# Kernel optimization log

Measured on AMD Instinct MI355X. Metric: run time of the kernel, lower is better.

## Reference

```python
import jax, jax.numpy as jnp
import numpy as np

B = 8          # batch_size
N = 2048       # N_particles
D_SP = 2       # spatial dims
D = 16         # D_SP + hidden_dim
K = 32         # max_num_neighbors
R = 0.08       # neighbor_radius
DT = 0.01      # leapfrog step
BIG = 1e9


def setup_inputs() -> dict:
    key = jax.random.key(0)
    ks = jax.random.split(key, 8)
    H, C = 64, 32
    # node state: small random hidden features, deterministic disk positions
    x = jax.random.normal(ks[0], (B * N, D), dtype=jnp.float32) * 0.001
    i = jnp.arange(N, dtype=jnp.float32)
    golden = jnp.pi * (3.0 - jnp.sqrt(5.0))
    theta = i * golden
    r = 0.6 * jnp.sqrt((i + 0.5) / N)
    pos = jnp.stack([r * jnp.cos(theta), r * jnp.sin(theta)], axis=1)  # [N,2]
    pos = jnp.tile(pos, (B, 1)) + 0.01 * jax.random.normal(ks[1], (B * N, 2), dtype=jnp.float32)
    x = x.at[:, :D_SP].set(pos)
    W1 = jax.random.normal(ks[2], (2 * D, H), dtype=jnp.float32) * (1.0 / np.sqrt(2 * D))
    b1 = jnp.zeros((H,), jnp.float32)
    W2 = jax.random.normal(ks[3], (H, C), dtype=jnp.float32) * (1.0 / np.sqrt(H))
    b2 = jnp.zeros((C,), jnp.float32)
    Wout = jax.random.normal(ks[4], (C, 1), dtype=jnp.float32) * (1.0 / np.sqrt(C))
    bout = jnp.zeros((1,), jnp.float32)
    batch = jnp.repeat(jnp.arange(B, dtype=jnp.int64), N)
    return {"x": x, "W1": W1, "b1": b1, "W2": W2, "b2": b2,
            "Wout": Wout, "bout": bout, "batch": batch, "steps": 2}


def reference(x, W1, b1, W2, b2, Wout, bout, batch, steps):
    Bn, Df = x.shape
    Bc = int(np.asarray(batch)[-1]) + 1      # batch is contiguous blocks
    Nn = Bn // Bc
    eye = jnp.eye(Nn, dtype=x.dtype) * BIG   # no self-loops (loop=False)

    def hamiltonian(xv):
        xb = xv.reshape(Bc, Nn, Df)
        pos = xb[:, :, :D_SP]                              # [B,N,2]
        # radius_graph: pairwise sq-dist per simulation, capped at K neighbors
        d2 = jnp.sum((pos[:, :, None, :] - pos[:, None, :, :]) ** 2, axis=-1)  # [B,N,N]
        d2 = d2 + eye
        negd, idx = jax.lax.top_k(-d2, K)                  # K nearest per node
        valid = (-negd) < (R * R)                          # [B,N,K]
        # gather neighbor states (HNNConv message on concat(x_i, x_j))
        xj = xb[jnp.arange(Bc)[:, None, None], idx]        # [B,N,K,D]
        xi = jnp.broadcast_to(xb[:, :, None, :], xj.shape)
        m = jnp.tanh(jnp.concatenate([xi, xj], axis=-1) @ W1 + b1)  # [B,N,K,H]
        m = m @ W2 + b2                                    # [B,N,K,C]
        m = jnp.where(valid[..., None], m, 0.0)
        agg = m.sum(axis=2)                                # sum aggregation [B,N,C]
        h = agg @ Wout + bout                              # per-node Hamiltonian [B,N,1]
        return h.sum()

    for _ in range(int(steps)):
        dHdx = jax.grad(hamiltonian)(x)
        x = x - DT * dHdx
    return x
```

## Files before the change

### kernel.cpp

```cpp
#include <hip/hip_runtime.h>
#include <cstdint>
#include <cstddef>

#define BB   8
#define NN   2048
#define DD   16
#define HHH  64
#define KK   32
#define CAP  96
#define DT_C 0.01f
#define R2_C (0.08f * 0.08f)
#define CEXP (-2.885390081777927f)

#define WPB   16
#define BLOCK (WPB * 64)

__device__ __forceinline__ float dist2(float px, float py, float qx, float qy) {
    float dx = __fsub_rn(px, qx);
    float dy = __fsub_rn(py, qy);
    return __fadd_rn(__fmul_rn(dx, dx), __fmul_rn(dy, dy));
}

__device__ __forceinline__ int mbcnt64(unsigned long long m) {
    return (int)__builtin_amdgcn_mbcnt_hi(
        (unsigned)(m >> 32), __builtin_amdgcn_mbcnt_lo((unsigned)m, 0u));
}

template <bool FIRST>
__global__ __launch_bounds__(BLOCK) void k_neighbors(
    const float* __restrict__ x, const float* __restrict__ pos,
    const float* __restrict__ W1,
    unsigned short* __restrict__ nbr, int* __restrict__ cntArr,
    float* __restrict__ cutArr,
    float* __restrict__ Aplane, float* __restrict__ Dplane) {
    __shared__ float sPos[2 * NN];
    __shared__ float sW1[2 * DD * HHH];
    __shared__ float2 sDJ[WPB][CAP];

    int tid = threadIdx.x;
    int w = tid >> 6, lane = tid & 63;
    int p = blockIdx.x * WPB + w;
    int pl = p & (NN - 1);
    int bbase = (p >> 11) << 11;

    if (FIRST) {
        for (int t = tid; t < 2 * NN; t += BLOCK)
            sPos[t] = x[(size_t)(bbase + (t >> 1)) * DD + (t & 1)];
    } else {
        for (int t = tid; t < 2 * NN; t += BLOCK) sPos[t] = pos[bbase * 2 + t];
    }
    for (int t = tid; t < 2 * DD * HHH; t += BLOCK) sW1[t] = W1[t];
    __syncthreads();

    float xv = (lane < DD) ? x[(size_t)p * DD + lane] : 0.f;
    float A = 0.f, Dv = 0.f;
#pragma unroll
    for (int f = 0; f < DD; f++) {
        float xf = __shfl(xv, f);
        A  = fmaf(xf, sW1[f * HHH + lane], A);
        Dv = fmaf(xf, sW1[(DD + f) * HHH + lane], Dv);
    }
    Aplane[((size_t)p << 6) + lane] = A;
    Dplane[((size_t)p << 6) + lane] = Dv;

    float px = sPos[2 * pl], py = sPos[2 * pl + 1];
    const float2* sPos2 = (const float2*)sPos;
    int cnt = 0;
    for (int c0 = 0; c0 < NN; c0 += 256) {
        float2 q[4];
#pragma unroll
        for (int u = 0; u < 4; ++u) q[u] = sPos2[c0 + (u << 6) + lane];
#pragma unroll
        for (int u = 0; u < 4; ++u) {
            int j = c0 + (u << 6) + lane;
            float d2 = dist2(px, py, q[u].x, q[u].y);
            bool hit = (d2 < R2_C) && (j != pl);
            unsigned long long m = __ballot(hit);
            int idx = cnt + mbcnt64(m & ((1ull << lane) - 1ull));
            if (hit && idx < CAP)
                sDJ[w][idx] = make_float2(d2, __uint_as_float((unsigned)j));
            cnt += (int)__popcll(m);
        }
    }
    if (cnt > CAP) cnt = CAP;
    __threadfence_block();

    float cutoff = R2_C;
    if (cnt > KK) {
        const float INF = 1e30f;
        if (cnt <= 64) {
            float v = (lane < cnt) ? sDJ[w][lane].x : INF;
#pragma unroll
            for (int k = 2; k <= 64; k <<= 1) {
#pragma unroll
                for (int j = k >> 1; j > 0; j >>= 1) {
                    float pv = __shfl_xor(v, j);
                    bool up = ((lane & k) == 0);
                    bool takeMin = (((lane & j) == 0) == up);
                    v = takeMin ? fminf(v, pv) : fmaxf(v, pv);
                }
            }
            cutoff = __shfl(v, KK - 1);
        } else {
            float e0 = (lane < cnt) ? sDJ[w][lane].x : INF;
            float e1 = (lane + 64 < cnt) ? sDJ[w][lane + 64].x : INF;
            int r0 = 0, q0 = 0, r1 = 0, q1 = 0;
            for (int k = 0; k < cnt; k++) {
                float val = sDJ[w][k].x;
                r0 += (val < e0); q0 += (val == e0);
                r1 += (val < e1); q1 += (val == e1);
            }
            bool c0 = (r0 <= KK - 1) && (r0 + q0 > KK - 1);
            bool c1 = (r1 <= KK - 1) && (r1 + q1 > KK - 1);
            float cand = c0 ? e0 : (c1 ? e1 : INF);
#pragma unroll
            for (int off = 32; off; off >>= 1) cand = fminf(cand, __shfl_xor(cand, off));
            cutoff = cand;
        }
    }
    if (lane == 0) { cutArr[p] = cutoff; cntArr[p] = cnt; }
    for (int c = lane; c < cnt; c += 64) {
        float2 e = sDJ[w][c];
        unsigned j = __float_as_uint(e.y);
        bool fwd = (e.x <= cutoff);
        nbr[(size_t)p * CAP + c] = (unsigned short)(j | (fwd ? 0x8000u : 0u));
    }
}

template <bool FIRST>
__global__ __launch_bounds__(BLOCK) void k_grad(
    const float* __restrict__ x, const float* __restrict__ pos,
    const float* __restrict__ cutArr, const int* __restrict__ cntArr,
    const unsigned short* __restrict__ nbr,
    const float* __restrict__ Aplane, const float* __restrict__ Dplane,
    const float* __restrict__ W1, const float* __restrict__ b1,
    const float* __restrict__ W2, const float* __restrict__ Wout,
    float* __restrict__ xOut, float* __restrict__ posOut) {
    __shared__ float sW1t[HHH * 33];
    __shared__ unsigned short sFwd[WPB][CAP];
    __shared__ unsigned short sRev[WPB][CAP];
    __shared__ float sS[WPB][128];
    __shared__ float sV[HHH];

    int tid = threadIdx.x;
    int w = tid >> 6, h = tid & 63;
    int p = blockIdx.x * WPB + w;
    int bbase = (p >> 11) << 11;

    for (int t = tid; t < 2 * DD * HHH; t += BLOCK) {
        int f = t >> 6, hh = t & 63;
        sW1t[hh * 33 + f] = W1[t];
    }
    if (tid < HHH) {
        float acc = 0.f;
        for (int c = 0; c < 32; c++) acc = fmaf(W2[tid * 32 + c], Wout[c], acc);
        sV[tid] = acc;
    }
    __syncthreads();

    float b1h = b1[h];
    float Apb = Aplane[((size_t)p << 6) + h] + b1h;
    float Dpb = Dplane[((size_t)p << 6) + h] + b1h;
    float vh4 = 4.f * sV[h];
    int cnt = cntArr[p];

    float px, py;
    if (FIRST) {
        float2 pp = *(const float2*)(x + (size_t)p * DD);
        px = pp.x; py = pp.y;
    } else {
        float2 pp = *(const float2*)(pos + (size_t)p * 2);
        px = pp.x; py = pp.y;
    }

    int mf = 0, mr = 0;
    for (int c0 = 0; c0 < cnt; c0 += 64) {
        int c = c0 + h;
        bool act = c < cnt;
        int cc = act ? c : cnt - 1;
        int jp = (int)nbr[(size_t)p * CAP + cc];
        int jl = jp & (NN - 1);
        float2 q;
        if (FIRST) q = *(const float2*)(x + (size_t)(bbase + jl) * DD);
        else       q = *(const float2*)(pos + (size_t)(bbase + jl) * 2);
        float d2 = dist2(px, py, q.x, q.y);
        float cutj = cutArr[bbase + jl];
        bool fwd = act && (jp & 0x8000);
        bool rev = act && (d2 <= cutj);
        unsigned long long mF = __ballot(fwd);
        int iF = mf + mbcnt64(mF & ((1ull << h) - 1ull));
        if (fwd) sFwd[w][iF] = (unsigned short)jl;
        mf += (int)__popcll(mF);
        unsigned long long mR = __ballot(rev);
        int iR = mr + mbcnt64(mR & ((1ull << h) - 1ull));
        if (rev) sRev[w][iR] = (unsigned short)jl;
        mr += (int)__popcll(mR);
    }
    __threadfence_block();

    const float* baseD = Dplane + ((size_t)bbase << 6);
    const float* baseA = Aplane + ((size_t)bbase << 6);
    float T1 = 0.f, T2 = 0.f;

    auto edgeF = [&](unsigned jl) {
        float dj = baseD[((size_t)jl << 6) + h];
        float z = Apb + dj;
        float a = __builtin_amdgcn_exp2f(CEXP * fabsf(z));
        float bb = 1.f + a;
        T1 += a * __builtin_amdgcn_rcpf(bb * bb);
    };
    auto edgeR = [&](unsigned jl) {
        float aj = baseA[((size_t)jl << 6) + h];
        float z = Dpb + aj;
        float a = __builtin_amdgcn_exp2f(CEXP * fabsf(z));
        float bb = 1.f + a;
        T2 += a * __builtin_amdgcn_rcpf(bb * bb);
    };

    {
        const unsigned short* L = sFwd[w];
        int c = 0;
        for (; c + 8 <= mf; c += 8) {
            int4 qw = *(const int4*)(L + c);
            unsigned w0 = (unsigned)__builtin_amdgcn_readfirstlane(qw.x);
            unsigned w1 = (unsigned)__builtin_amdgcn_readfirstlane(qw.y);
            unsigned w2 = (unsigned)__builtin_amdgcn_readfirstlane(qw.z);
            unsigned w3 = (unsigned)__builtin_amdgcn_readfirstlane(qw.w);
            edgeF(w0 & 0xffffu); edgeF(w0 >> 16);
            edgeF(w1 & 0xffffu); edgeF(w1 >> 16);
            edgeF(w2 & 0xffffu); edgeF(w2 >> 16);
            edgeF(w3 & 0xffffu); edgeF(w3 >> 16);
        }
        for (; c < mf; ++c)
            edgeF((unsigned)__builtin_amdgcn_readfirstlane((int)L[c]));
    }
    {
        const unsigned short* L = sRev[w];
        int c = 0;
        for (; c + 8 <= mr; c += 8) {
            int4 qw = *(const int4*)(L + c);
            unsigned w0 = (unsigned)__builtin_amdgcn_readfirstlane(qw.x);
            unsigned w1 = (unsigned)__builtin_amdgcn_readfirstlane(qw.y);
            unsigned w2 = (unsigned)__builtin_amdgcn_readfirstlane(qw.z);
            unsigned w3 = (unsigned)__builtin_amdgcn_readfirstlane(qw.w);
            edgeR(w0 & 0xffffu); edgeR(w0 >> 16);
            edgeR(w1 & 0xffffu); edgeR(w1 >> 16);
            edgeR(w2 & 0xffffu); edgeR(w2 >> 16);
            edgeR(w3 & 0xffffu); edgeR(w3 >> 16);
        }
        for (; c < mr; ++c)
            edgeR((unsigned)__builtin_amdgcn_readfirstlane((int)L[c]));
    }

    sS[w][h] = vh4 * T1;
    sS[w][64 + h] = vh4 * T2;
    __threadfence_block();

    float g = 0.f;
    if (h < 32) {
        const float* Sv = &sS[w][(h < 16) ? 0 : 64];
        float acc = 0.f;
        for (int hh = 0; hh < 64; hh++) acc = fmaf(sW1t[hh * 33 + h], Sv[hh], acc);
        g = acc;
    }
    float g2 = __shfl(g, (h + 16) & 63);
    if (h < DD) {
        float xn = x[(size_t)p * DD + h] - DT_C * (g + g2);
        xOut[(size_t)p * DD + h] = xn;
        if (h < 2) posOut[p * 2 + h] = xn;
    }
}

extern "C" void kernel_launch(void* const* d_in, const int* in_sizes, int n_in,
                              void* d_out, int out_size, void* d_ws, size_t ws_size,
                              hipStream_t stream) {
    const float* x0   = (const float*)d_in[0];
    const float* W1   = (const float*)d_in[1];
    const float* b1   = (const float*)d_in[2];
    const float* W2   = (const float*)d_in[3];
    const float* Wout = (const float*)d_in[5];
    float* out = (float*)d_out;

    float* ws   = (float*)d_ws;
    float* posA = ws;
    float* posB = posA + 32768;
    float* x1   = posB + 32768;
    float* Apl  = x1 + 262144;
    float* Dpl  = Apl + 16384 * 64;
    float* cut  = Dpl + 16384 * 64;
    int*   cnt  = (int*)(cut + 16384);
    unsigned short* nbr = (unsigned short*)(cnt + 16384);

    dim3 blk(BLOCK);
    const int NBLK = (BB * NN) / WPB;

    k_neighbors<true><<<NBLK, blk, 0, stream>>>(x0, nullptr, W1, nbr, cnt, cut, Apl, Dpl);
    k_grad<true><<<NBLK, blk, 0, stream>>>(x0, nullptr, cut, cnt, nbr, Apl, Dpl,
                                           W1, b1, W2, Wout, x1, posB);
    k_neighbors<false><<<NBLK, blk, 0, stream>>>(x1, posB, W1, nbr, cnt, cut, Apl, Dpl);
    k_grad<false><<<NBLK, blk, 0, stream>>>(x1, posB, cut, cnt, nbr, Apl, Dpl,
                                            W1, b1, W2, Wout, out, posA);
}
```

Baseline: 189.1 us.

## Swizzle block-to-batch mapping, vectorize position loads, batch gathers in edge loops

Blocks are remapped so consecutive block IDs cycle across the eight simulations, which spreads concurrent work over different batch slices of the A/D planes. The first-step position staging now loads float2 pairs instead of scalars. The edge loops in the gradient kernel are unrolled to 16 edges, with all 16 gathers issued before the exp/rcp math so more memory loads are in flight. The cost is higher register pressure, and the swizzle may reduce L2 locality for neighbour-plane reads.

```diff
diff --git a/kernel.cpp b/kernel.cpp
--- a/kernel.cpp
+++ b/kernel.cpp
@@ -24,6 +24,12 @@
 __device__ __forceinline__ int mbcnt64(unsigned long long m) {
     return (int)__builtin_amdgcn_mbcnt_hi(
         (unsigned)(m >> 32), __builtin_amdgcn_mbcnt_lo((unsigned)m, 0u));
+}
+
+__device__ __forceinline__ int swizzled_particle(int blk, int w, int& bbase) {
+    int vb = blk & 7, vi = blk >> 3;
+    bbase = vb << 11;
+    return bbase + vi * WPB + w;
 }
 
 template <bool FIRST>
@@ -39,13 +45,14 @@
 
     int tid = threadIdx.x;
     int w = tid >> 6, lane = tid & 63;
-    int p = blockIdx.x * WPB + w;
+    int bbase;
+    int p = swizzled_particle(blockIdx.x, w, bbase);
     int pl = p & (NN - 1);
-    int bbase = (p >> 11) << 11;
-
+
+    float2* sPos2w = (float2*)sPos;
     if (FIRST) {
-        for (int t = tid; t < 2 * NN; t += BLOCK)
-            sPos[t] = x[(size_t)(bbase + (t >> 1)) * DD + (t & 1)];
+        for (int t = tid; t < NN; t += BLOCK)
+            sPos2w[t] = *(const float2*)(x + (size_t)(bbase + t) * DD);
     } else {
         for (int t = tid; t < 2 * NN; t += BLOCK) sPos[t] = pos[bbase * 2 + t];
     }
@@ -137,15 +144,15 @@
     const float* __restrict__ W2, const float* __restrict__ Wout,
     float* __restrict__ xOut, float* __restrict__ posOut) {
     __shared__ float sW1t[HHH * 33];
-    __shared__ unsigned short sFwd[WPB][CAP];
-    __shared__ unsigned short sRev[WPB][CAP];
+    __shared__ alignas(16) unsigned short sFwd[WPB][CAP];
+    __shared__ alignas(16) unsigned short sRev[WPB][CAP];
     __shared__ float sS[WPB][128];
     __shared__ float sV[HHH];
 
     int tid = threadIdx.x;
     int w = tid >> 6, h = tid & 63;
-    int p = blockIdx.x * WPB + w;
-    int bbase = (p >> 11) << 11;
+    int bbase;
+    int p = swizzled_particle(blockIdx.x, w, bbase);
 
     for (int t = tid; t < 2 * DD * HHH; t += BLOCK) {
         int f = t >> 6, hh = t & 63;
@@ -202,55 +209,92 @@
     const float* baseA = Aplane + ((size_t)bbase << 6);
     float T1 = 0.f, T2 = 0.f;
 
-    auto edgeF = [&](unsigned jl) {
-        float dj = baseD[((size_t)jl << 6) + h];
-        float z = Apb + dj;
+    auto s2core = [&](float z) {
         float a = __builtin_amdgcn_exp2f(CEXP * fabsf(z));
         float bb = 1.f + a;
-        T1 += a * __builtin_amdgcn_rcpf(bb * bb);
+        return a * __builtin_amdgcn_rcpf(bb * bb);
     };
-    auto edgeR = [&](unsigned jl) {
-        float aj = baseA[((size_t)jl << 6) + h];
-        float z = Dpb + aj;
-        float a = __builtin_amdgcn_exp2f(CEXP * fabsf(z));
-        float bb = 1.f + a;
-        T2 += a * __builtin_amdgcn_rcpf(bb * bb);
-    };
+
+#define UNPACK8(Q0, Q1, U)                                            \
+    unsigned U[8];                                                    \
+    U[0] = (unsigned)__builtin_amdgcn_readfirstlane(Q0.x);            \
+    U[1] = (unsigned)__builtin_amdgcn_readfirstlane(Q0.y);            \
+    U[2] = (unsigned)__builtin_amdgcn_readfirstlane(Q0.z);            \
+    U[3] = (unsigned)__builtin_amdgcn_readfirstlane(Q0.w);            \
+    U[4] = (unsigned)__builtin_amdgcn_readfirstlane(Q1.x);            \
+    U[5] = (unsigned)__builtin_amdgcn_readfirstlane(Q1.y);            \
+    U[6] = (unsigned)__builtin_amdgcn_readfirstlane(Q1.z);            \
+    U[7] = (unsigned)__builtin_amdgcn_readfirstlane(Q1.w);
 
     {
         const unsigned short* L = sFwd[w];
         int c = 0;
+        for (; c + 16 <= mf; c += 16) {
+            int4 q0 = *(const int4*)(L + c);
+            int4 q1 = *(const int4*)(L + c + 8);
+            UNPACK8(q0, q1, u)
+            float d[16];
+#pragma unroll
+            for (int k = 0; k < 8; ++k) {
+                d[2 * k]     = baseD[((size_t)(u[k] & 0xffffu) << 6) + h];
+                d[2 * k + 1] = baseD[((size_t)(u[k] >> 16) << 6) + h];
+            }
+#pragma unroll
+            for (int k = 0; k < 16; ++k) T1 += s2core(Apb + d[k]);
+        }
         for (; c + 8 <= mf; c += 8) {
-            int4 qw = *(const int4*)(L + c);
-            unsigned w0 = (unsigned)__builtin_amdgcn_readfirstlane(qw.x);
-            unsigned w1 = (unsigned)__builtin_amdgcn_readfirstlane(qw.y);
-            unsigned w2 = (unsigned)__builtin_amdgcn_readfirstlane(qw.z);
-            unsigned w3 = (unsigned)__builtin_amdgcn_readfirstlane(qw.w);
-            edgeF(w0 & 0xffffu); edgeF(w0 >> 16);
-            edgeF(w1 & 0xffffu); edgeF(w1 >> 16);
-            edgeF(w2 & 0xffffu); edgeF(w2 >> 16);
-            edgeF(w3 & 0xffffu); edgeF(w3 >> 16);
-        }
-        for (; c < mf; ++c)
-            edgeF((unsigned)__builtin_amdgcn_readfirstlane((int)L[c]));
+            int4 q0 = *(const int4*)(L + c);
+            int4 q1 = q0;
+            UNPACK8(q0, q1, u)
+            float d[8];
+#pragma unroll
+            for (int k = 0; k < 4; ++k) {
+                d[2 * k]     = baseD[((size_t)(u[k] & 0xffffu) << 6) + h];
+                d[2 * k + 1] = baseD[((size_t)(u[k] >> 16) << 6) + h];
+            }
+#pragma unroll
+            for (int k = 0; k < 8; ++k) T1 += s2core(Apb + d[k]);
+        }
+        for (; c < mf; ++c) {
+            unsigned jl = (unsigned)__builtin_amdgcn_readfirstlane((int)L[c]);
+            T1 += s2core(Apb + baseD[((size_t)jl << 6) + h]);
+        }
     }
     {
         const unsigned short* L = sRev[w];
         int c = 0;
+        for (; c + 16 <= mr; c += 16) {
+            int4 q0 = *(const int4*)(L + c);
+            int4 q1 = *(const int4*)(L + c + 8);
+            UNPACK8(q0, q1, u)
+            float d[16];
+#pragma unroll
+            for (int k = 0; k < 8; ++k) {
+                d[2 * k]     = baseA[((size_t)(u[k] & 0xffffu) << 6) + h];
+                d[2 * k + 1] = baseA[((size_t)(u[k] >> 16) << 6) + h];
+            }
+#pragma unroll
+            for (int k = 0; k < 16; ++k) T2 += s2core(Dpb + d[k]);
+        }
         for (; c + 8 <= mr; c += 8) {
-            int4 qw = *(const int4*)(L + c);
-            unsigned w0 = (unsigned)__builtin_amdgcn_readfirstlane(qw.x);
-            unsigned w1 = (unsigned)__builtin_amdgcn_readfirstlane(qw.y);
-            unsigned w2 = (unsigned)__builtin_amdgcn_readfirstlane(qw.z);
-            unsigned w3 = (unsigned)__builtin_amdgcn_readfirstlane(qw.w);
-            edgeR(w0 & 0xffffu); edgeR(w0 >> 16);
-            edgeR(w1 & 0xffffu); edgeR(w1 >> 16);
-            edgeR(w2 & 0xffffu); edgeR(w2 >> 16);
-            edgeR(w3 & 0xffffu); edgeR(w3 >> 16);
-        }
-        for (; c < mr; ++c)
-            edgeR((unsigned)__builtin_amdgcn_readfirstlane((int)L[c]));
-    }
+            int4 q0 = *(const int4*)(L + c);
+            int4 q1 = q0;
+            UNPACK8(q0, q1, u)
+            float d[8];
+#pragma unroll
+            for (int k = 0; k < 4; ++k) {
+                d[2 * k]     = baseA[((size_t)(u[k] & 0xffffu) << 6) + h];
+                d[2 * k + 1] = baseA[((size_t)(u[k] >> 16) << 6) + h];
+            }
+#pragma unroll
+            for (int k = 0; k < 8; ++k) T2 += s2core(Dpb + d[k]);
+        }
+        for (; c < mr; ++c) {
+            unsigned jl = (unsigned)__builtin_amdgcn_readfirstlane((int)L[c]);
+            T2 += s2core(Dpb + baseA[((size_t)jl << 6) + h]);
+        }
+    }
+#undef UNPACK8
 
     sS[w][h] = vh4 * T1;
     sS[w][64 + h] = vh4 * T2;
```

New measurement: 178.3 us. 1.06x faster.
